# Kernel optimization log

Hardware: AMD Instinct MI355X
Metric: run time of the kernel (lower is better)

The kernel has to match this reference:

```python
import jax, jax.numpy as jnp
import numpy as np
import math
from jax import lax

S = 2048   # layer_size (number of neurons)
T = 384    # timesteps per forward call
ALPHA = 0.15
DT = 0.1
THRESH = -50.0
V_RESET = -70.0
VL = -70.0
GL = 0.025
CM = 0.5
TAU = CM / GL                                   # 20.0
COEF = DT ** ALPHA * math.gamma(2.0 - ALPHA) / CM  # dt^alpha * Gamma(2-alpha) / Cm


def setup_inputs() -> dict:
    key = jax.random.key(0)
    I_old = jax.random.normal(key, (S, T), dtype=jnp.float32)
    # class-level fractional (Grunwald-Letnikov style) weight vector, x=5000
    x = 5000
    nv = np.arange(x - 1)
    w = ((x - nv + 1) ** (1.0 - ALPHA) - (x - nv) ** (1.0 - ALPHA)).astype(np.float32)
    return {"I_old": I_old, "weights": jnp.asarray(w)}


def _forward(I_old, weights):
    S_, T_ = I_old.shape
    dtype = I_old.dtype
    # wr[a] = weights[-a]: the memory weight applied to a delta that is `a` steps old.
    # Original: np.inner(weights[-N+1:], delta_trace) pairs oldest delta with weights[-(N-1)]
    # and the newest delta with weights[-1].
    wr = jnp.concatenate([jnp.zeros((1,), dtype), weights[::-1][:T_].astype(dtype)])  # [T+1]
    jidx = jnp.arange(T_)  # buffer slot j holds the delta appended at global step j

    def step(carry, xs):
        V, buf = carry          # V: [S], buf: [S, T] delta history (slot j = delta of step j)
        n, I_n = xs             # n: scalar step index, I_n: [S]
        # fractional memory term: sum_{j=1}^{n-1} wr[n-j] * delta_j
        ages = n - jidx                                        # [T]
        coeff = jnp.where((ages >= 1) & (jidx >= 1),
                          wr[jnp.clip(ages, 0, T_)], jnp.zeros((), dtype))  # [T]
        memory = buf @ coeff                                   # [S]
        # three update rules depending on the global step counter
        V1 = V + (DT / TAU) * (-V + I_n / GL)                  # N == 1 branch
        V2 = COEF * (-GL * (V - VL) + I_n) + V - memory        # N >= 2 branch
        V_pre = jnp.where(n == 0, jnp.full_like(V, -70.0),
                          jnp.where(n == 1, V1, V2))
        spike = (V - THRESH > 0).astype(dtype)                 # spike uses PREVIOUS V
        reset = lax.stop_gradient(spike * (THRESH - V_RESET))  # detached reset
        V_new = V_pre - reset
        buf = buf.at[:, n].set(V_new - V)                      # append delta (n=0 slot masked out)
        return (V_new, buf), (spike, V_new)

    V0 = jnp.zeros((S_,), dtype)          # V_trace initialized to 0 per neuron
    buf0 = jnp.zeros((S_, T_), dtype)
    (_, _), (spk, trc) = lax.scan(step, (V0, buf0), (jnp.arange(T_), I_old.T))
    return spk.T, trc.T                    # each [S, T]


def reference(I_old, weights):
    return _forward(I_old, weights)
```

## Files before the change

kernel.cpp:

```cpp
#include <hip/hip_runtime.h>
#include <cmath>

#define T_STEPS 384
#define CH 64
#define NCH 6
#define WS 392

__device__ __forceinline__ float readlane_f(float v, int l) {
    return __int_as_float(__builtin_amdgcn_readlane(__float_as_int(v), l));
}

__global__ __launch_bounds__(64, 2)
void flif_kernel(const float* __restrict__ I_old, const float* __restrict__ W,
                 float* __restrict__ out, float cm1, float c2, float c3, int Stot)
{
    const int s    = blockIdx.x;
    const int lane = threadIdx.x;

    __shared__ __align__(16) float wtr[4 * WS];
    __shared__ __align__(16) float lrep[4 * 128];
    __shared__ __align__(16) float dbuf[T_STEPS];

    const float* Irow = I_old + (size_t)s * T_STEPS;
    float Inext = Irow[lane];

    #pragma unroll
    for (int r = 0; r < 4; ++r) {
        for (int k = lane; k < WS; k += 64) {
            const int i = k + r;
            wtr[r * WS + k] = (i <= 382) ? W[4998 - i] : 0.0f;
        }
        for (int k = lane; k < 128; k += 64) {
            const int x = k + r;
            lrep[r * 128 + k] = (x >= 64 && x <= 126) ? W[5062 - x] : 0.0f;
        }
    }
    __syncthreads();

    float wloc[64];
    {
        const int r = lane & 3;
        const float* lp = lrep + r * 128 - r;
        #pragma unroll
        for (int i0 = 0; i0 < 64; i0 += 4) {
            const float4 f = *reinterpret_cast<const float4*>(lp + (lane + 60 - i0));
            wloc[i0 + 0] = f.w; wloc[i0 + 1] = f.z;
            wloc[i0 + 2] = f.y; wloc[i0 + 3] = f.x;
        }
    }

    const int rl = lane & 3;
    const float* wlp = wtr + rl * WS + (lane - rl);

    float* out_spk = out + (size_t)s * T_STEPS;
    float* out_trc = out + (size_t)Stot * T_STEPS + (size_t)s * T_STEPS;

    const float wr1n = -W[4998];

    float V = 0.0f, d = 0.0f, b = 0.0f, P = 0.0f;

    for (int c = 0; c < NCH; ++c) {
        const int cb = c * CH;
        const float Ic = Inext;
        if (c + 1 < NCH) Inext = Irow[cb + CH + lane];

        float acc = 0.0f;
        #pragma unroll 4
        for (int m0 = cb - 4; m0 >= 0; m0 -= 4) {
            const float4 d4 = *reinterpret_cast<const float4*>(dbuf + (cb - m0 - 4));
            const float4 w4 = *reinterpret_cast<const float4*>(wlp + m0);
            acc = fmaf(d4.x, w4.w, acc);
            acc = fmaf(d4.y, w4.z, acc);
            acc = fmaf(d4.z, w4.y, acc);
            acc = fmaf(d4.w, w4.x, acc);
        }

        float u = fmaf(c3, Ic, c2) - acc;
        const float Vs = V;
        float tc = 0.0f;

        auto body = [&](int i) {
            const float t = fmaf(wr1n, d, P);
            d = t + b;
            P = readlane_f(u, (i + 1) & 63);
            V = V + d;
            const float rv = (V > -50.0f) ? -20.0f : 0.0f;
            b = fmaf(cm1, V, rv);
            u = fmaf(-wloc[i], d, u);
            tc = (lane == i) ? V : tc;
        };

        if (c == 0) {
            V = -90.0f;
            if (lane == 0) tc = V;
            const float I1 = readlane_f(Ic, 1);
            const float V1 = fmaf(0.005f, (I1 / 0.025f) - V, V);
            const float d1 = V1 - V;
            P = readlane_f(u, 2);
            u = fmaf(-wloc[1], d1, u);
            if (lane == 1) tc = V1;
            V = V1;
            d = d1;
            const float rv = (V > -50.0f) ? -20.0f : 0.0f;
            b = fmaf(cm1, V, rv);
            #pragma unroll
            for (int i = 2; i < CH; ++i) body(i);
        } else {
            d = 0.0f;
            P = readlane_f(u, 0);
            #pragma unroll
            for (int i = 0; i < CH; ++i) body(i);
        }

        float prev = __shfl_up(tc, 1);
        if (lane == 0) prev = Vs;
        const float spk = (prev > -50.0f) ? 1.0f : 0.0f;
        float dd = tc - prev;
        if (c == 0 && lane == 0) dd = 0.0f;
        dbuf[cb + lane] = dd;
        out_spk[cb + lane] = spk;
        out_trc[cb + lane] = tc;
    }
}

extern "C" void kernel_launch(void* const* d_in, const int* in_sizes, int n_in,
                              void* d_out, int out_size, void* d_ws, size_t ws_size,
                              hipStream_t stream) {
    const float* I = (const float*)d_in[0];
    const float* W = (const float*)d_in[1];
    float* out = (float*)d_out;
    const int S = in_sizes[0] / T_STEPS;

    const double COEF = std::pow(0.1, 0.15) * std::tgamma(1.85) / 0.5;
    const float c3  = (float)COEF;
    const float cm1 = (float)(-COEF * 0.025);
    const float c2  = (float)(COEF * 0.025 * -70.0);

    flif_kernel<<<S, 64, 0, stream>>>(I, W, out, cm1, c2, c3, S);
}
```

Baseline: 85.72 us.

## Add helper wavefront to precompute older-history memory sums concurrently with serial recurrence

Launches a second wavefront per neuron that, while the main wave runs the serial 64-step recurrence for chunk c, computes the long-history dot product for chunk c+1 over all but the most recent chunk. The result is handed over through a double-buffered shared array. The main wave then only adds the most recent chunk's contribution. Output stores are deferred to the end of the kernel. This shortens the critical path per chunk, at the cost of a __syncthreads per chunk, double the threads per block, and more register pressure from holding the outputs.

```diff
diff --git a/kernel.cpp b/kernel.cpp
--- a/kernel.cpp
+++ b/kernel.cpp
@@ -10,32 +10,59 @@
     return __int_as_float(__builtin_amdgcn_readlane(__float_as_int(v), l));
 }
 
-__global__ __launch_bounds__(64, 2)
+__global__ __launch_bounds__(128, 4)
 void flif_kernel(const float* __restrict__ I_old, const float* __restrict__ W,
                  float* __restrict__ out, float cm1, float c2, float c3, int Stot)
 {
+    const int tid  = threadIdx.x;
+    const int wid  = tid >> 6;
+    const int lane = tid & 63;
     const int s    = blockIdx.x;
-    const int lane = threadIdx.x;
 
     __shared__ __align__(16) float wtr[4 * WS];
     __shared__ __align__(16) float lrep[4 * 128];
     __shared__ __align__(16) float dbuf[T_STEPS];
+    __shared__ float accs[2][CH];
+
+    for (int k = tid; k < 4 * WS; k += 128) {
+        const int r = k / WS, kk = k - r * WS;
+        const int i = kk + r;
+        wtr[k] = (i <= 382) ? W[4998 - i] : 0.0f;
+    }
+    for (int k = tid; k < 512; k += 128) {
+        const int r = k >> 7, kk = k & 127;
+        const int x = kk + r;
+        lrep[k] = (x >= 64 && x <= 126) ? W[5062 - x] : 0.0f;
+    }
+    ((float*)accs)[tid] = 0.0f;
+    __syncthreads();
+
+    const int rl = lane & 3;
+    const float* wlp = wtr + rl * WS + (lane - rl);
+
+    if (wid == 1) {
+        for (int c = 0; c < NCH; ++c) {
+            if (c >= 1 && c <= 4) {
+                const int CB = (c + 1) * CH;
+                float acc = 0.0f;
+                #pragma unroll 2
+                for (int m0 = CB - 4; m0 >= 64; m0 -= 4) {
+                    const float4 d4 = *reinterpret_cast<const float4*>(dbuf + (CB - m0 - 4));
+                    const float4 w4 = *reinterpret_cast<const float4*>(wlp + m0);
+                    acc = fmaf(d4.x, w4.w, acc);
+                    acc = fmaf(d4.y, w4.z, acc);
+                    acc = fmaf(d4.z, w4.y, acc);
+                    acc = fmaf(d4.w, w4.x, acc);
+                }
+                accs[(c + 1) & 1][lane] = acc;
+            }
+            __syncthreads();
+        }
+        return;
+    }
 
     const float* Irow = I_old + (size_t)s * T_STEPS;
     float Inext = Irow[lane];
-
-    #pragma unroll
-    for (int r = 0; r < 4; ++r) {
-        for (int k = lane; k < WS; k += 64) {
-            const int i = k + r;
-            wtr[r * WS + k] = (i <= 382) ? W[4998 - i] : 0.0f;
-        }
-        for (int k = lane; k < 128; k += 64) {
-            const int x = k + r;
-            lrep[r * 128 + k] = (x >= 64 && x <= 126) ? W[5062 - x] : 0.0f;
-        }
-    }
-    __syncthreads();
 
     float wloc[64];
     {
@@ -49,30 +76,27 @@
         }
     }
 
-    const int rl = lane & 3;
-    const float* wlp = wtr + rl * WS + (lane - rl);
-
-    float* out_spk = out + (size_t)s * T_STEPS;
-    float* out_trc = out + (size_t)Stot * T_STEPS + (size_t)s * T_STEPS;
-
     const float wr1n = -W[4998];
 
     float V = 0.0f, d = 0.0f, b = 0.0f, P = 0.0f;
+    float tcs[NCH], spks[NCH];
 
     for (int c = 0; c < NCH; ++c) {
         const int cb = c * CH;
         const float Ic = Inext;
         if (c + 1 < NCH) Inext = Irow[cb + CH + lane];
 
-        float acc = 0.0f;
-        #pragma unroll 4
-        for (int m0 = cb - 4; m0 >= 0; m0 -= 4) {
-            const float4 d4 = *reinterpret_cast<const float4*>(dbuf + (cb - m0 - 4));
-            const float4 w4 = *reinterpret_cast<const float4*>(wlp + m0);
-            acc = fmaf(d4.x, w4.w, acc);
-            acc = fmaf(d4.y, w4.z, acc);
-            acc = fmaf(d4.z, w4.y, acc);
-            acc = fmaf(d4.w, w4.x, acc);
+        float acc = accs[c & 1][lane];
+        if (c >= 1) {
+            #pragma unroll 2
+            for (int m0 = 60; m0 >= 0; m0 -= 4) {
+                const float4 d4 = *reinterpret_cast<const float4*>(dbuf + (cb - m0 - 4));
+                const float4 w4 = *reinterpret_cast<const float4*>(wlp + m0);
+                acc = fmaf(d4.x, w4.w, acc);
+                acc = fmaf(d4.y, w4.z, acc);
+                acc = fmaf(d4.z, w4.y, acc);
+                acc = fmaf(d4.w, w4.x, acc);
+            }
         }
 
         float u = fmaf(c3, Ic, c2) - acc;
@@ -114,12 +138,20 @@
 
         float prev = __shfl_up(tc, 1);
         if (lane == 0) prev = Vs;
-        const float spk = (prev > -50.0f) ? 1.0f : 0.0f;
+        spks[c] = (prev > -50.0f) ? 1.0f : 0.0f;
         float dd = tc - prev;
         if (c == 0 && lane == 0) dd = 0.0f;
         dbuf[cb + lane] = dd;
-        out_spk[cb + lane] = spk;
-        out_trc[cb + lane] = tc;
+        tcs[c] = tc;
+        __syncthreads();
+    }
+
+    float* out_spk = out + (size_t)s * T_STEPS;
+    float* out_trc = out + (size_t)Stot * T_STEPS + (size_t)s * T_STEPS;
+    #pragma unroll
+    for (int c = 0; c < NCH; ++c) {
+        out_spk[c * CH + lane] = spks[c];
+        out_trc[c * CH + lane] = tcs[c];
     }
 }
 
@@ -136,5 +168,5 @@
     const float cm1 = (float)(-COEF * 0.025);
     const float c2  = (float)(COEF * 0.025 * -70.0);
 
-    flif_kernel<<<S, 64, 0, stream>>>(I, W, out, cm1, c2, c3, S);
+    flif_kernel<<<S, 128, 0, stream>>>(I, W, out, cm1, c2, c3, S);
 }
```

New measurement: 85.09 us. About the same (-0.7%).
